# Kernel tuning notes

Hardware: AMD Instinct MI355X
Metric: run time of the kernel (lower is better)

The kernel has to match this reference:

```python
import jax, jax.numpy as jnp
import numpy as np

LN_EPS = 1e-5


def _layernorm(x, g, b):
    mu = jnp.mean(x, axis=-1, keepdims=True)
    var = jnp.mean(jnp.square(x - mu), axis=-1, keepdims=True)
    return (x - mu) * jax.lax.rsqrt(var + LN_EPS) * g + b


def setup_inputs() -> dict:
    key = jax.random.key(0)
    ks = jax.random.split(key, 4)
    B, N, C = 32, 512, 1024
    return {
        "r": jax.random.normal(ks[0], (B, N, C), dtype=jnp.float32),
        "ln_gamma": jnp.ones((C,), dtype=jnp.float32),
        "ln_beta": jnp.zeros((C,), dtype=jnp.float32),
        "qkv_w": jax.random.normal(ks[1], (C, 3 * C), dtype=jnp.float32) * (C ** -0.5),
        "qkv_b": jnp.zeros((3 * C,), dtype=jnp.float32),
        "proj_w": jax.random.normal(ks[2], (C, C), dtype=jnp.float32) * (C ** -0.5),
        "proj_b": jnp.zeros((C,), dtype=jnp.float32),
        "sig_w": jax.random.normal(ks[3], (C, C), dtype=jnp.float32) * (C ** -0.5),
        "sig_b": jnp.zeros((C,), dtype=jnp.float32),
        "num_heads": 16,
        "latent_num": 64,
    }


def reference(r, ln_gamma, ln_beta, qkv_w, qkv_b, proj_w, proj_b, sig_w, sig_b,
              num_heads, latent_num):
    B, N, C = r.shape
    H = num_heads
    D = C // H
    scale = D ** -0.5

    x = _layernorm(r, ln_gamma, ln_beta)
    qkv = (x @ qkv_w + qkv_b).reshape(B, N, 3, H, D)
    q, k, v = jnp.moveaxis(qkv, 2, 0)              # each (B, N, H, D)
    q = jnp.transpose(q, (0, 2, 1, 3))             # (B, H, N, D)
    k = jnp.transpose(k, (0, 2, 1, 3))
    v = jnp.transpose(v, (0, 2, 1, 3))

    attn = jax.nn.softmax(jnp.einsum('bhnd,bhmd->bhnm', q, k) * scale, axis=-1)
    out = jnp.einsum('bhnm,bhmd->bhnd', attn, v)   # (B, H, N, D)
    out = jnp.transpose(out, (0, 2, 1, 3)).reshape(B, N, C)
    out = out @ proj_w + proj_b

    out = out + out                                 # r + DropPath(r), eval -> Identity
    agg = jnp.mean(out, axis=1)                     # (B, C)
    mu = jnp.mean(agg, axis=0, keepdims=True)       # (1, C)
    sigma = 0.1 + 0.9 * jax.nn.sigmoid(mu @ sig_w + sig_b)  # (1, C)

    eps = jax.random.normal(jax.random.key(42), (latent_num, 1, C), dtype=r.dtype)
    latent = jnp.squeeze(mu + sigma * eps, axis=1)  # (latent_num, C)
    return latent
```

## Files before the change

kernel.cpp:

```cpp
#include <hip/hip_runtime.h>

#define B_ 32
#define N_ 512
#define C_ 1024
#define H_ 16
#define D_ 64
#define TC_ 3072
#define NQK_ 2048
#define M_ (B_*N_)

typedef unsigned int u32;
typedef unsigned short u16;
typedef __attribute__((ext_vector_type(8))) unsigned short ushort8;
typedef __attribute__((ext_vector_type(8))) short bf16x8;
typedef __attribute__((ext_vector_type(4))) float f32x4;

__device__ __forceinline__ float bfl(u32 u){ return __builtin_bit_cast(float, u << 16); }
__device__ __forceinline__ u16 f2bf(float f){
  u32 u = __builtin_bit_cast(u32, f);
  u32 r = (u + 0x7FFFu + ((u >> 16) & 1u)) >> 16;
  return (u16)r;
}

__global__ __launch_bounds__(256) void k_pre(const float* __restrict__ r,
                                             const float* __restrict__ g,
                                             const float* __restrict__ be,
                                             const float* __restrict__ W,
                                             u16* __restrict__ X,
                                             u16* __restrict__ WT) {
  __shared__ float tile[32][33];
  int bid = blockIdx.x, t = threadIdx.x;
  if (bid < M_) {
    float* red = &tile[0][0];
    int row = bid;
    float4 v = ((const float4*)(r + (size_t)row * C_))[t];
    float s = (v.x + v.y) + (v.z + v.w);
    #pragma unroll
    for (int o = 32; o; o >>= 1) s += __shfl_xor(s, o);
    if ((t & 63) == 0) red[t >> 6] = s;
    __syncthreads();
    float mean = (red[0] + red[1] + red[2] + red[3]) * (1.f / 1024.f);
    float d0 = v.x - mean, d1 = v.y - mean, d2 = v.z - mean, d3 = v.w - mean;
    float q = d0*d0 + d1*d1 + d2*d2 + d3*d3;
    #pragma unroll
    for (int o = 32; o; o >>= 1) q += __shfl_xor(q, o);
    if ((t & 63) == 0) red[4 + (t >> 6)] = q;
    __syncthreads();
    float var = (red[4] + red[5] + red[6] + red[7]) * (1.f / 1024.f);
    float rs = rsqrtf(var + 1e-5f);
    float4 gv = ((const float4*)g)[t];
    float4 bv = ((const float4*)be)[t];
    ushort4 o4;
    o4.x = f2bf(d0 * rs * gv.x + bv.x);
    o4.y = f2bf(d1 * rs * gv.y + bv.y);
    o4.z = f2bf(d2 * rs * gv.z + bv.z);
    o4.w = f2bf(d3 * rs * gv.w + bv.w);
    ((ushort4*)X)[(size_t)row * 256 + t] = o4;
  } else {
    int wb = bid - M_;
    int k0 = (wb & 31) * 32, n0 = (wb >> 5) * 32;
    int rr = t >> 3, c4 = (t & 7) * 4;
    float4 v = *(const float4*)(W + (size_t)(k0 + rr) * TC_ + n0 + c4);
    tile[rr][c4] = v.x; tile[rr][c4 + 1] = v.y; tile[rr][c4 + 2] = v.z; tile[rr][c4 + 3] = v.w;
    __syncthreads();
    int n = t >> 3, k4 = (t & 7) * 4;
    ushort4 o;
    o.x = f2bf(tile[k4][n]);     o.y = f2bf(tile[k4 + 1][n]);
    o.z = f2bf(tile[k4 + 2][n]); o.w = f2bf(tile[k4 + 3][n]);
    *(ushort4*)(WT + (size_t)(n0 + n) * C_ + k0 + k4) = o;
  }
}

__global__ __launch_bounds__(256) void k_qk(const u16* __restrict__ X,
                                            const u16* __restrict__ WT,
                                            const float* __restrict__ bias,
                                            u16* __restrict__ QK) {
  __shared__ u16 As[128 * 32];
  __shared__ u16 Bs[128 * 32];
  int t = threadIdx.x, lane = t & 63, w = t >> 6;
  int wr = w >> 1, wc = w & 1;
  int bid = blockIdx.x;
  int swz = (bid & 7) * 256 + (bid >> 3);
  int rowA0 = (swz >> 4) * 128, colB0 = (swz & 15) * 128;
  int colbase = lane & 15, kslot = lane >> 4;

  f32x4 acc[4][4] = {};

  for (int k0 = 0; k0 < C_; k0 += 32) {
    __syncthreads();
    const u16* Xrow = X + (size_t)rowA0 * C_ + k0;
    const u16* Wrow = WT + (size_t)colB0 * C_ + k0;
    #pragma unroll
    for (int p = 0; p < 2; p++) {
      int o = p * 4096 + w * 1024 + lane * 16;
      int row = o >> 6, slot = (o >> 4) & 3;
      int kb16 = slot ^ ((row >> 1) & 3);
      const u16* gp = Xrow + (size_t)row * C_ + (kb16 << 3);
      __builtin_amdgcn_global_load_lds((const __attribute__((address_space(1))) void*)gp,
                                       (__attribute__((address_space(3))) void*)((char*)As + o),
                                       16, 0, 0);
    }
    #pragma unroll
    for (int p = 0; p < 2; p++) {
      int o = p * 4096 + w * 1024 + lane * 16;
      int row = o >> 6, slot = (o >> 4) & 3;
      int kb16 = slot ^ ((row >> 1) & 3);
      const u16* gp = Wrow + (size_t)row * C_ + (kb16 << 3);
      __builtin_amdgcn_global_load_lds((const __attribute__((address_space(1))) void*)gp,
                                       (__attribute__((address_space(3))) void*)((char*)Bs + o),
                                       16, 0, 0);
    }
    __syncthreads();
    bf16x8 a[4], b[4];
    #pragma unroll
    for (int i = 0; i < 4; i++) {
      int row = wr * 64 + i * 16 + colbase;
      a[i] = *(const bf16x8*)((const char*)As + row * 64 + ((kslot ^ ((row >> 1) & 3)) << 4));
    }
    #pragma unroll
    for (int j = 0; j < 4; j++) {
      int col = wc * 64 + j * 16 + colbase;
      b[j] = *(const bf16x8*)((const char*)Bs + col * 64 + ((kslot ^ ((col >> 1) & 3)) << 4));
    }
    #pragma unroll
    for (int i = 0; i < 4; i++)
      #pragma unroll
      for (int j = 0; j < 4; j++)
        acc[i][j] = __builtin_amdgcn_mfma_f32_16x16x32_bf16(a[i], b[j], acc[i][j], 0, 0, 0);
  }

  float bv[4];
  #pragma unroll
  for (int j = 0; j < 4; j++) bv[j] = bias[colB0 + wc * 64 + j * 16 + colbase];
  #pragma unroll
  for (int i = 0; i < 4; i++) {
    #pragma unroll
    for (int j = 0; j < 4; j++) {
      int col = colB0 + wc * 64 + j * 16 + colbase;
      int tsel = col >> 10, rem = col & 1023;
      int h = rem >> 6, dd = rem & 63;
      #pragma unroll
      for (int q = 0; q < 4; q++) {
        int m = rowA0 + wr * 64 + i * 16 + (lane >> 4) * 4 + q;
        int b2 = m >> 9, n = m & 511;
        QK[(((size_t)(tsel * B_ + b2) * H_ + h) * N_ + n) * D_ + dd] = f2bf(acc[i][j][q] + bv[j]);
      }
    }
  }
}

__global__ __launch_bounds__(512) void k_attn(const u16* __restrict__ QK,
                                              float* __restrict__ CWg) {
  __shared__ u16 Ks[N_ * D_];
  __shared__ float rsl[N_];
  int bh = blockIdx.x;
  const u16* qb = QK + (size_t)bh * (N_ * D_);
  const u16* kb = QK + (size_t)(B_ * H_ + bh) * (N_ * D_);
  int t = threadIdx.x, lane = t & 63, w = t >> 6;
  int colbase = lane & 15, kslot = lane >> 4;

  #pragma unroll
  for (int i2 = 0; i2 < 8; i2++) {
    int vec = t + i2 * 512;
    int c = vec >> 3, d8 = vec & 7;
    uint4 pk = *(const uint4*)(kb + ((size_t)c << 6) + (d8 << 3));
    *(uint4*)((char*)Ks + c * 128 + ((d8 ^ (c & 7)) << 4)) = pk;
  }
  __syncthreads();

  #pragma unroll 1
  for (int si = 0; si < 4; si++) {
    int n0 = (w * 4 + si) * 16;
    bf16x8 aq0 = *(const bf16x8*)(qb + (size_t)(n0 + colbase) * 64 + kslot * 8);
    bf16x8 aq1 = *(const bf16x8*)(qb + (size_t)(n0 + colbase) * 64 + 32 + kslot * 8);
    float sj[4] = {0.f, 0.f, 0.f, 0.f};
    #pragma unroll 4
    for (int tl = 0; tl < 32; tl++) {
      int m = tl * 16 + colbase;
      const char* kr = (const char*)Ks + m * 128;
      bf16x8 bk0 = *(const bf16x8*)(kr + ((kslot ^ (m & 7)) << 4));
      bf16x8 bk1 = *(const bf16x8*)(kr + (((kslot + 4) ^ (m & 7)) << 4));
      f32x4 z = {0.f, 0.f, 0.f, 0.f};
      z = __builtin_amdgcn_mfma_f32_16x16x32_bf16(aq0, bk0, z, 0, 0, 0);
      z = __builtin_amdgcn_mfma_f32_16x16x32_bf16(aq1, bk1, z, 0, 0, 0);
      #pragma unroll
      for (int q = 0; q < 4; q++) sj[q] += __expf(z[q] * 0.125f);
    }
    #pragma unroll
    for (int q = 0; q < 4; q++) {
      sj[q] += __shfl_xor(sj[q], 1);
      sj[q] += __shfl_xor(sj[q], 2);
      sj[q] += __shfl_xor(sj[q], 4);
      sj[q] += __shfl_xor(sj[q], 8);
    }
    if (colbase == 0) {
      #pragma unroll
      for (int q = 0; q < 4; q++) rsl[n0 + kslot * 4 + q] = 1.f / sj[q];
    }
  }
  __syncthreads();

  bf16x8 kf[4][2];
  #pragma unroll
  for (int ct = 0; ct < 4; ct++) {
    int m = (w * 4 + ct) * 16 + colbase;
    const char* kr = (const char*)Ks + m * 128;
    kf[ct][0] = *(const bf16x8*)(kr + ((kslot ^ (m & 7)) << 4));
    kf[ct][1] = *(const bf16x8*)(kr + (((kslot + 4) ^ (m & 7)) << 4));
  }
  f32x4 acc[4] = {};
  #pragma unroll 2
  for (int si = 0; si < 32; si++) {
    int n0 = si * 16;
    bf16x8 aq0 = *(const bf16x8*)(qb + (size_t)(n0 + colbase) * 64 + kslot * 8);
    bf16x8 aq1 = *(const bf16x8*)(qb + (size_t)(n0 + colbase) * 64 + 32 + kslot * 8);
    float rr = rsl[n0 + colbase];
    #pragma unroll
    for (int ct = 0; ct < 4; ct++) {
      f32x4 z = {0.f, 0.f, 0.f, 0.f};
      z = __builtin_amdgcn_mfma_f32_16x16x32_bf16(kf[ct][0], aq0, z, 0, 0, 0);
      z = __builtin_amdgcn_mfma_f32_16x16x32_bf16(kf[ct][1], aq1, z, 0, 0, 0);
      #pragma unroll
      for (int q = 0; q < 4; q++) acc[ct][q] += __expf(z[q] * 0.125f) * rr;
    }
  }
  #pragma unroll
  for (int ct = 0; ct < 4; ct++) {
    #pragma unroll
    for (int q = 0; q < 4; q++) {
      float v = acc[ct][q];
      v += __shfl_xor(v, 1);
      v += __shfl_xor(v, 2);
      v += __shfl_xor(v, 4);
      v += __shfl_xor(v, 8);
      if (colbase == 0)
        CWg[(size_t)bh * 512 + (w * 4 + ct) * 16 + kslot * 4 + q] = v * (1.f / 512.f);
    }
  }
}

__global__ __launch_bounds__(256) void k_ybar(const float* __restrict__ CW,
                                              const u16* __restrict__ X,
                                              float* __restrict__ Y2) {
  __shared__ float cwl[256][17];
  int bid = blockIdx.x;
  int kb = bid & 7, b = (bid >> 3) & 31, mh = bid >> 8;
  int t = threadIdx.x;
  int h = t >> 4, ks = t & 15;
  int m0 = mh * 256;
  #pragma unroll
  for (int i = 0; i < 16; i++)
    cwl[t][i] = CW[(size_t)(b * 16 + i) * 512 + m0 + t];
  __syncthreads();
  int kc = kb * 128 + ks * 8;
  const u16* Xb = X + ((size_t)b * 512 + m0) * 1024 + kc;
  float acc[8] = {};
  #pragma unroll 4
  for (int m = 0; m < 256; m++) {
    float wgt = cwl[m][h];
    ushort8 xv = *(const ushort8*)(Xb + (size_t)m * 1024);
    #pragma unroll
    for (int e = 0; e < 8; e++) acc[e] = fmaf(wgt, bfl((u32)xv[e]), acc[e]);
  }
  float* yp = Y2 + ((size_t)(mh * 32 + b) * 16 + h) * 1024 + kc;
  *(float4*)yp = *(float4*)&acc[0];
  *(float4*)(yp + 4) = *(float4*)&acc[4];
}

__global__ __launch_bounds__(256) void k_head0(const float* __restrict__ y,
                                               const float* __restrict__ qkvw,
                                               const float* __restrict__ qkvb,
                                               float* __restrict__ z) {
  __shared__ float yb[1024];
  __shared__ float part[4][64];
  int h = blockIdx.x, t = threadIdx.x;
  for (int k = t; k < 1024; k += 256) {
    float s = 0.f;
    #pragma unroll 4
    for (int p = 0; p < 64; p++) s += y[((size_t)(p * 16 + h) << 10) + k];
    yb[k] = s * (1.f / 32.f);
  }
  __syncthreads();
  int col = t & 63, q = t >> 6;
  float acc = 0.f;
  for (int k = q * 256; k < q * 256 + 256; k++)
    acc = fmaf(yb[k], qkvw[(size_t)k * TC_ + 2048 + h * 64 + col], acc);
  part[q][col] = acc;
  __syncthreads();
  if (t < 64)
    z[h * 64 + t] = part[0][t] + part[1][t] + part[2][t] + part[3][t] + qkvb[2048 + h * 64 + t];
}

__global__ __launch_bounds__(256) void k_head1(const float* __restrict__ z,
                                               const float* __restrict__ pw,
                                               const float* __restrict__ pb,
                                               float* __restrict__ mu) {
  __shared__ float zs[1024];
  __shared__ float part[8][32];
  int t = threadIdx.x;
  for (int j = t; j < 1024; j += 256) zs[j] = z[j];
  __syncthreads();
  int col = blockIdx.x * 32 + (t & 31), q = t >> 5;
  float acc = 0.f;
  #pragma unroll 4
  for (int k = q * 128; k < q * 128 + 128; k++)
    acc = fmaf(zs[k], pw[(size_t)k * 1024 + col], acc);
  part[q][t & 31] = acc;
  __syncthreads();
  if (t < 32) {
    float s = pb[blockIdx.x * 32 + t];
    #pragma unroll
    for (int p = 0; p < 8; p++) s += part[p][t];
    mu[blockIdx.x * 32 + t] = 2.f * s;
  }
}

__global__ __launch_bounds__(256) void k_head2(const float* __restrict__ mu,
                                               const float* __restrict__ sw,
                                               const float* __restrict__ sb,
                                               float* __restrict__ sig) {
  __shared__ float ms[1024];
  __shared__ float part[8][32];
  int t = threadIdx.x;
  for (int j = t; j < 1024; j += 256) ms[j] = mu[j];
  __syncthreads();
  int col = blockIdx.x * 32 + (t & 31), q = t >> 5;
  float acc = 0.f;
  #pragma unroll 4
  for (int k = q * 128; k < q * 128 + 128; k++)
    acc = fmaf(ms[k], sw[(size_t)k * 1024 + col], acc);
  part[q][t & 31] = acc;
  __syncthreads();
  if (t < 32) {
    float s = sb[blockIdx.x * 32 + t];
    #pragma unroll
    for (int p = 0; p < 8; p++) s += part[p][t];
    sig[blockIdx.x * 32 + t] = 0.1f + 0.9f / (1.f + expf(-s));
  }
}

__device__ __forceinline__ uint2 threefry_0_42(u32 x0, u32 x1) {
  const u32 ks0 = 0u, ks1 = 42u, ks2 = 0x1BD11BF0u;
  x0 += ks0; x1 += ks1;
  #define RND(r) { x0 += x1; x1 = (x1 << r) | (x1 >> (32 - r)); x1 ^= x0; }
  RND(13) RND(15) RND(26) RND(6)   x0 += ks1; x1 += ks2 + 1u;
  RND(17) RND(29) RND(16) RND(24)  x0 += ks2; x1 += ks0 + 2u;
  RND(13) RND(15) RND(26) RND(6)   x0 += ks0; x1 += ks1 + 3u;
  RND(17) RND(29) RND(16) RND(24)  x0 += ks1; x1 += ks2 + 4u;
  RND(13) RND(15) RND(26) RND(6)   x0 += ks2; x1 += ks0 + 5u;
  #undef RND
  return make_uint2(x0, x1);
}

__device__ __forceinline__ float bits_to_normal(u32 bits) {
  u32 fb = (bits >> 9) | 0x3F800000u;
  float fl = __builtin_bit_cast(float, fb) - 1.0f;
  float u = __fmul_rn(fl, 2.0f);
  u = __fadd_rn(u, -0.99999994f);
  u = fmaxf(-0.99999994f, u);
  float x = u;
  float wv = -log1pf(-x * x);
  float p;
  if (wv < 5.0f) {
    wv -= 2.5f;
    p = 2.81022636e-08f;
    p = fmaf(p, wv, 3.43273939e-07f);
    p = fmaf(p, wv, -3.5233877e-06f);
    p = fmaf(p, wv, -4.39150654e-06f);
    p = fmaf(p, wv, 0.00021858087f);
    p = fmaf(p, wv, -0.00125372503f);
    p = fmaf(p, wv, -0.00417768164f);
    p = fmaf(p, wv, 0.246640727f);
    p = fmaf(p, wv, 1.50140941f);
  } else {
    wv = sqrtf(wv) - 3.0f;
    p = -0.000200214257f;
    p = fmaf(p, wv, 0.000100950558f);
    p = fmaf(p, wv, 0.00134934322f);
    p = fmaf(p, wv, -0.00367342844f);
    p = fmaf(p, wv, 0.00573950773f);
    p = fmaf(p, wv, -0.0076224613f);
    p = fmaf(p, wv, 0.00943887047f);
    p = fmaf(p, wv, 1.00167406f);
    p = fmaf(p, wv, 2.83297682f);
  }
  return 1.41421356f * (p * x);
}

__global__ __launch_bounds__(256) void k_latent(const float* __restrict__ mu,
                                                const float* __restrict__ sig,
                                                float* __restrict__ out) {
  u32 f = blockIdx.x * 256 + threadIdx.x;
  uint2 rb = threefry_0_42(0u, f);
  float eps = bits_to_normal(rb.x ^ rb.y);
  int c = f & 1023;
  out[f] = mu[c] + sig[c] * eps;
}

extern "C" void kernel_launch(void* const* d_in, const int* in_sizes, int n_in,
                              void* d_out, int out_size, void* d_ws, size_t ws_size,
                              hipStream_t stream) {
  const float* r    = (const float*)d_in[0];
  const float* lng  = (const float*)d_in[1];
  const float* lnb  = (const float*)d_in[2];
  const float* qkvw = (const float*)d_in[3];
  const float* qkvb = (const float*)d_in[4];
  const float* pw   = (const float*)d_in[5];
  const float* pb   = (const float*)d_in[6];
  const float* sw   = (const float*)d_in[7];
  const float* sb   = (const float*)d_in[8];
  float* out = (float*)d_out;

  u16* X   = (u16*)d_ws;
  u16* QK  = X + (size_t)M_ * C_;
  u16* WT  = QK + (size_t)2 * M_ * C_;
  float* CW = (float*)(WT + (size_t)NQK_ * C_);
  float* Y2 = CW + (size_t)B_ * H_ * N_;
  float* Z  = Y2 + (size_t)64 * H_ * C_;
  float* MU  = Z + C_;
  float* SIG = MU + C_;

  k_pre<<<M_ + NQK_, 256, 0, stream>>>(r, lng, lnb, qkvw, X, WT);
  k_qk<<<M_ / 128 * (NQK_ / 128), 256, 0, stream>>>(X, WT, qkvb, QK);
  k_attn<<<B_ * H_, 512, 0, stream>>>(QK, CW);
  k_ybar<<<512, 256, 0, stream>>>(CW, X, Y2);
  k_head0<<<H_, 256, 0, stream>>>(Y2, qkvw, qkvb, Z);
  k_head1<<<32, 256, 0, stream>>>(Z, pw, pb, MU);
  k_head2<<<32, 256, 0, stream>>>(MU, sw, sb, SIG);
  k_latent<<<256, 256, 0, stream>>>(MU, SIG, out);
}
```

Measured before the change: 262.4 us.

## Drop K shared-memory staging and hold four Q tiles in registers

Removes the 64KB shared-memory copy of K and its barrier, so K fragments are read straight from global memory (L1/L2). The row-sum pass now keeps four Q tiles in registers and reuses each loaded K tile across all four, instead of looping over Q tiles with K re-read from LDS. Freeing the LDS should let more blocks fit per CU. The cost is uncoalesced 16-byte global loads of K repeated by every wave, plus higher register pressure.

Result: slower. 272.8 us (+4.0%).

```diff
diff --git a/kernel.cpp b/kernel.cpp
--- a/kernel.cpp
+++ b/kernel.cpp
@@ -151,7 +151,6 @@
 
 __global__ __launch_bounds__(512) void k_attn(const u16* __restrict__ QK,
                                               float* __restrict__ CWg) {
-  __shared__ u16 Ks[N_ * D_];
   __shared__ float rsl[N_];
   int bh = blockIdx.x;
   const u16* qb = QK + (size_t)bh * (N_ * D_);
@@ -159,43 +158,38 @@
   int t = threadIdx.x, lane = t & 63, w = t >> 6;
   int colbase = lane & 15, kslot = lane >> 4;
 
-  #pragma unroll
-  for (int i2 = 0; i2 < 8; i2++) {
-    int vec = t + i2 * 512;
-    int c = vec >> 3, d8 = vec & 7;
-    uint4 pk = *(const uint4*)(kb + ((size_t)c << 6) + (d8 << 3));
-    *(uint4*)((char*)Ks + c * 128 + ((d8 ^ (c & 7)) << 4)) = pk;
-  }
-  __syncthreads();
-
-  #pragma unroll 1
+  bf16x8 aq[4][2];
+  #pragma unroll
   for (int si = 0; si < 4; si++) {
     int n0 = (w * 4 + si) * 16;
-    bf16x8 aq0 = *(const bf16x8*)(qb + (size_t)(n0 + colbase) * 64 + kslot * 8);
-    bf16x8 aq1 = *(const bf16x8*)(qb + (size_t)(n0 + colbase) * 64 + 32 + kslot * 8);
-    float sj[4] = {0.f, 0.f, 0.f, 0.f};
-    #pragma unroll 4
-    for (int tl = 0; tl < 32; tl++) {
-      int m = tl * 16 + colbase;
-      const char* kr = (const char*)Ks + m * 128;
-      bf16x8 bk0 = *(const bf16x8*)(kr + ((kslot ^ (m & 7)) << 4));
-      bf16x8 bk1 = *(const bf16x8*)(kr + (((kslot + 4) ^ (m & 7)) << 4));
+    aq[si][0] = *(const bf16x8*)(qb + (size_t)(n0 + colbase) * 64 + kslot * 8);
+    aq[si][1] = *(const bf16x8*)(qb + (size_t)(n0 + colbase) * 64 + 32 + kslot * 8);
+  }
+  f32x4 sj[4] = {};
+  #pragma unroll 2
+  for (int tl = 0; tl < 32; tl++) {
+    int m = tl * 16 + colbase;
+    bf16x8 bk0 = *(const bf16x8*)(kb + (size_t)m * 64 + kslot * 8);
+    bf16x8 bk1 = *(const bf16x8*)(kb + (size_t)m * 64 + 32 + kslot * 8);
+    #pragma unroll
+    for (int si = 0; si < 4; si++) {
       f32x4 z = {0.f, 0.f, 0.f, 0.f};
-      z = __builtin_amdgcn_mfma_f32_16x16x32_bf16(aq0, bk0, z, 0, 0, 0);
-      z = __builtin_amdgcn_mfma_f32_16x16x32_bf16(aq1, bk1, z, 0, 0, 0);
+      z = __builtin_amdgcn_mfma_f32_16x16x32_bf16(aq[si][0], bk0, z, 0, 0, 0);
+      z = __builtin_amdgcn_mfma_f32_16x16x32_bf16(aq[si][1], bk1, z, 0, 0, 0);
       #pragma unroll
-      for (int q = 0; q < 4; q++) sj[q] += __expf(z[q] * 0.125f);
-    }
+      for (int q = 0; q < 4; q++) sj[si][q] += __expf(z[q] * 0.125f);
+    }
+  }
+  #pragma unroll
+  for (int si = 0; si < 4; si++) {
     #pragma unroll
     for (int q = 0; q < 4; q++) {
-      sj[q] += __shfl_xor(sj[q], 1);
-      sj[q] += __shfl_xor(sj[q], 2);
-      sj[q] += __shfl_xor(sj[q], 4);
-      sj[q] += __shfl_xor(sj[q], 8);
-    }
-    if (colbase == 0) {
-      #pragma unroll
-      for (int q = 0; q < 4; q++) rsl[n0 + kslot * 4 + q] = 1.f / sj[q];
+      float v = sj[si][q];
+      v += __shfl_xor(v, 1);
+      v += __shfl_xor(v, 2);
+      v += __shfl_xor(v, 4);
+      v += __shfl_xor(v, 8);
+      if (colbase == 0) rsl[(w * 4 + si) * 16 + kslot * 4 + q] = 1.f / v;
     }
   }
   __syncthreads();
@@ -204,9 +198,8 @@
   #pragma unroll
   for (int ct = 0; ct < 4; ct++) {
     int m = (w * 4 + ct) * 16 + colbase;
-    const char* kr = (const char*)Ks + m * 128;
-    kf[ct][0] = *(const bf16x8*)(kr + ((kslot ^ (m & 7)) << 4));
-    kf[ct][1] = *(const bf16x8*)(kr + (((kslot + 4) ^ (m & 7)) << 4));
+    kf[ct][0] = *(const bf16x8*)(kb + (size_t)m * 64 + kslot * 8);
+    kf[ct][1] = *(const bf16x8*)(kb + (size_t)m * 64 + 32 + kslot * 8);
   }
   f32x4 acc[4] = {};
   #pragma unroll 2
```
